# Optimization experiments

Measured on AMD Instinct MI355X. Metric: run time of the kernel, lower is better.

## Reference

```python
import jax, jax.numpy as jnp
import numpy as np


def setup_inputs() -> dict:
    key = jax.random.key(0)
    ks = jax.random.split(key, 8)
    B, C, H, W = 8, 64, 64, 64
    C2 = C // 2
    return {
        "x": jax.random.normal(ks[0], (B, C, H, W), dtype=jnp.float32),
        "Wq": jax.random.normal(ks[1], (C2, C), dtype=jnp.float32) * 0.1,
        "bq": jax.random.normal(ks[2], (C2,), dtype=jnp.float32) * 0.01,
        "Wk": jax.random.normal(ks[3], (C2, C), dtype=jnp.float32) * 0.1,
        "bk": jax.random.normal(ks[4], (C2,), dtype=jnp.float32) * 0.01,
        "Wv": jax.random.normal(ks[5], (C, C), dtype=jnp.float32) * 0.1,
        "bv": jax.random.normal(ks[6], (C,), dtype=jnp.float32) * 0.01,
        "sigma": jnp.float32(1.0),
    }


def reference(x, Wq, bq, Wk, bk, Wv, bv, sigma):
    B, C, H, W = x.shape
    N = H * W
    xf = x.reshape(B, C, N)  # flatten spatial
    # 1x1 convs == per-pixel linear projections over channels
    q = jnp.einsum("oc,bcn->bon", Wq, xf) + bq[None, :, None]  # [B, C/2, N]
    k = jnp.einsum("oc,bcn->bon", Wk, xf) + bk[None, :, None]  # [B, C/2, N]
    v = jnp.einsum("oc,bcn->bon", Wv, xf) + bv[None, :, None]  # [B, C,   N]
    # pairwise squared L2 distance via expansion: |q|^2 + |k|^2 - 2 q.k
    q_sq = jnp.sum(q * q, axis=1)  # [B, N]
    k_sq = jnp.sum(k * k, axis=1)  # [B, N]
    qk = jnp.einsum("bcn,bcm->bnm", q, k)  # [B, N, N]
    dist_sq = q_sq[:, :, None] + k_sq[:, None, :] - 2.0 * qk
    similarity = jnp.exp(-dist_sq / (2.0 * sigma * sigma))  # RBF kernel
    attention = jax.nn.softmax(similarity, axis=-1)  # [B, N, N]
    # attn @ v^T -> [B, N, C]
    attention_out = jnp.einsum("bnm,bcm->bnc", attention, v)
    # faithful to torch .view(B, C, H, W) on a [B, N, C] tensor (raw reshape)
    attention_out = attention_out.reshape(B, C, H, W)
    return x + attention_out
```

## Files before the change

kernel.cpp:

```cpp
#include <hip/hip_runtime.h>
#include <hip/hip_bf16.h>

typedef __attribute__((ext_vector_type(2))) _Float16 f16x2;
typedef __attribute__((ext_vector_type(4))) _Float16 f16x4;
typedef __attribute__((ext_vector_type(8))) _Float16 f16x8;
typedef __attribute__((ext_vector_type(4))) float f32x4;

#define B_ 8
#define N_ 4096
#define C_ 64
#define CQ_ 32
#define SPLIT 4
#define KEYS (N_ / SPLIT)
#define MB 64
#define NT (KEYS / MB)
#define QB 128

#define L2E_ 1.4426950408889634f
#define LOG2L_ 0.5287663729448977f

#define P0_ 0.9992f
#define P1_ 0.70591f
#define P2_ 0.20093f
#define P3_ 0.094395f

__device__ __forceinline__ void async16(void* lds, const void* gsrc) {
    __builtin_amdgcn_global_load_lds(
        (const __attribute__((address_space(1))) unsigned int*)gsrc,
        (__attribute__((address_space(3))) unsigned int*)lds, 16, 0, 0);
}

__device__ __forceinline__ f16x2 wpoly(float z0, float z1) {
    f16x2 h = __builtin_bit_cast(f16x2, __builtin_amdgcn_cvt_pkrtz(z0, z1));
    const _Float16 c3 = (_Float16)P3_, c2 = (_Float16)P2_;
    const _Float16 c1 = (_Float16)P1_, c0 = (_Float16)P0_;
    return ((h * c3 + c2) * h + c1) * h + c0;
}

__global__ __launch_bounds__(256) void proj_kernel(
    const float* __restrict__ x,
    const float* __restrict__ Wq, const float* __restrict__ bq,
    const float* __restrict__ Wk, const float* __restrict__ bk,
    const float* __restrict__ Wv, const float* __restrict__ bv,
    const float* __restrict__ sigp,
    _Float16* __restrict__ qh, _Float16* __restrict__ khf,
    _Float16* __restrict__ vhf,
    float* __restrict__ nqs, float* __restrict__ nkf)
{
    __shared__ float xs[64][64];
    __shared__ float sP[4][64];
    __shared__ _Float16 vtmp[64][76];

    const int t = threadIdx.x;
    const int wid = __builtin_amdgcn_readfirstlane(t >> 6);
    const int l = t & 63;
    const int typeB = (int)(blockIdx.x >> 9);
    const int bid = blockIdx.x & 511;
    const int b = bid >> 6;
    const int tile = bid & 63;
    const int n0 = tile * 64;

    #pragma unroll
    for (int rep = 0; rep < 16; ++rep) {
        const int idx = rep * 256 + t;
        xs[idx >> 6][idx & 63] = x[((size_t)b * C_ + (idx >> 6)) * N_ + n0 + (idx & 63)];
    }
    __syncthreads();

    const float* Wr;
    const float* br;
    if (!typeB) {
        Wr = (wid < 2) ? (Wq + wid * 16 * 64) : (Wk + (wid - 2) * 16 * 64);
        br = (wid < 2) ? (bq + wid * 16) : (bk + (wid - 2) * 16);
    } else {
        Wr = Wv + wid * 16 * 64;
        br = bv + wid * 16;
    }

    float acc[16];
    #pragma unroll
    for (int o = 0; o < 16; ++o) acc[o] = br[o];
    #pragma unroll
    for (int c0 = 0; c0 < 64; c0 += 8) {
        float xc[8];
        #pragma unroll
        for (int dc = 0; dc < 8; ++dc) xc[dc] = xs[c0 + dc][l];
        #pragma unroll
        for (int o = 0; o < 16; ++o) {
            #pragma unroll
            for (int dc = 0; dc < 8; ++dc)
                acc[o] = fmaf(Wr[o * 64 + c0 + dc], xc[dc], acc[o]);
        }
    }

    const float sv = sigp[0];
    const float cdL = 0.7213475204444817f / (sv * sv);
    const float c1 = 2.0f * cdL;
    const int n = n0 + l;

    if (!typeB) {
        float s = 0.f;
        #pragma unroll
        for (int o = 0; o < 16; ++o) s = fmaf(acc[o], acc[o], s);
        sP[wid][l] = s;
        if (wid < 2) {
            _Float16* row = qh + ((size_t)b * N_ + n) * CQ_ + wid * 16;
            #pragma unroll
            for (int j = 0; j < 2; ++j) {
                f16x8 h;
                #pragma unroll
                for (int e = 0; e < 8; ++e) h[e] = (_Float16)(acc[j * 8 + e] * c1);
                *(f16x8*)(row + j * 8) = h;
            }
        } else {
            const size_t tbase = ((size_t)b * (N_ / 64) + tile) * 4;
            #pragma unroll
            for (int gi = 0; gi < 2; ++gi) {
                const int g = (wid - 2) * 2 + gi;
                f16x8 h;
                #pragma unroll
                for (int e = 0; e < 8; ++e) h[e] = (_Float16)acc[gi * 8 + e];
                *(f16x8*)(khf + (tbase + g) * 512 + l * 8) = h;
            }
        }
        __syncthreads();
        if (t < 64) {
            nqs[(size_t)b * N_ + n0 + t] = LOG2L_ - (sP[0][t] + sP[1][t]) * cdL;
        } else if (t < 128) {
            const int kk = t - 64;
            const int kap = (((kk & 15) >> 2) << 3) + (kk & 3) + (((kk >> 4) & 1) << 2);
            nkf[((size_t)b * (N_ / 32) + ((n0 + kk) >> 5)) * 32 + kap] =
                -(sP[2][kk] + sP[3][kk]) * cdL;
        }
    } else {
        #pragma unroll
        for (int o = 0; o < 16; ++o) vtmp[wid * 16 + o][l] = (_Float16)acc[o];
        __syncthreads();
        #pragma unroll
        for (int p = 0; p < 2; ++p) {
            const int jg = (t >> 6) + p * 4;
            const int ch = t & 63;
            const int p0 = (jg >> 2) * 32 + (jg & 3) * 4;
            const f16x4 a0 = *(const f16x4*)(&vtmp[ch][p0]);
            const f16x4 a1 = *(const f16x4*)(&vtmp[ch][p0 + 16]);
            f16x8 hv;
            #pragma unroll
            for (int e = 0; e < 4; ++e) { hv[e] = a0[e]; hv[4 + e] = a1[e]; }
            *(f16x8*)(vhf + ((size_t)b * (N_ / 64) + tile) * 4096 + (jg * 64 + ch) * 8) = hv;
        }
    }
}

__global__ __launch_bounds__(256, 4) void attn_kernel(
    const _Float16* __restrict__ qh,
    const _Float16* __restrict__ khf,
    const _Float16* __restrict__ vhf,
    const float* __restrict__ nqs,
    const float* __restrict__ nkf,
    _Float16* __restrict__ opart,
    float* __restrict__ dpart)
{
    __shared__ __align__(16) _Float16 Kb[3][2048];
    __shared__ __align__(16) _Float16 Vb[3][4096];
    __shared__ __align__(16) float sNkAll[1024];

    const int t = threadIdx.x;
    const int wid = t >> 6;
    const int l = t & 63;
    const int lg = l >> 4;
    const int lm = l & 15;

    const int orig = blockIdx.x;
    const int wgid = (orig & 7) * 128 + (orig >> 3);
    const int qblk = wgid & 31;
    const int fam = wgid >> 5;
    const int split = fam & (SPLIT - 1);
    const int b = fam >> 2;
    const int qbase = qblk * QB + wid * 32;
    const int k0 = split * KEYS;
    const size_t bN = (size_t)b * N_;

    const f16x8 qfA = *(const f16x8*)(qh + (bN + qbase + lm) * CQ_ + 8 * lg);
    const f16x8 qfB = *(const f16x8*)(qh + (bN + qbase + 16 + lm) * CQ_ + 8 * lg);
    const float nqA = nqs[bN + qbase + lm];
    const float nqB = nqs[bN + qbase + 16 + lm];

    const _Float16* kg = khf + ((size_t)b * (N_ / 64) + (k0 >> 6)) * 2048 + wid * 512 + l * 8;
    const _Float16* vg = vhf + ((size_t)b * (N_ / 64) + (k0 >> 6)) * 4096 + wid * 1024 + l * 8;
    const float* nkp = nkf + bN + k0 + wid * 256 + l * 4;

    f32x4 accA[4], accB[4], accdA, accdB;
    #pragma unroll
    for (int i = 0; i < 4; ++i) {
        accA[i] = (f32x4){0.f, 0.f, 0.f, 0.f};
        accB[i] = (f32x4){0.f, 0.f, 0.f, 0.f};
    }
    accdA = (f32x4){0.f, 0.f, 0.f, 0.f};
    accdB = (f32x4){0.f, 0.f, 0.f, 0.f};
    f16x8 ones;
    #pragma unroll
    for (int e = 0; e < 8; ++e) ones[e] = (_Float16)1.0f;

    f16x8 paJ0A, paJ0B, paJ1A, paJ1B;

    auto ISSUE = [&](int tile, int bf) {
        async16(&Kb[bf][wid * 512],        kg + (size_t)tile * 2048);
        async16(&Vb[bf][wid * 1024],       vg + (size_t)tile * 4096);
        async16(&Vb[bf][wid * 1024 + 512], vg + (size_t)tile * 4096 + 512);
    };

    auto HALF = [&](int J, int tt, int ck, int cv, bool doPV, f16x8& pA, f16x8& pB) {
        const f16x8 kf0 = *(const f16x8*)(&Kb[ck][(lg * 64 + J * 32 + lm) * 8]);
        const f16x8 kf1 = *(const f16x8*)(&Kb[ck][(lg * 64 + J * 32 + 16 + lm) * 8]);
        const f32x4 NK0 = *(const f32x4*)(&sNkAll[tt * 64 + J * 32 + lg * 8]);
        const f32x4 NK1 = *(const f32x4*)(&sNkAll[tt * 64 + J * 32 + lg * 8 + 4]);
        f32x4 CA0, CA1, CB0, CB1;
        #pragma unroll
        for (int r = 0; r < 4; ++r) {
            CA0[r] = NK0[r] + nqA; CA1[r] = NK1[r] + nqA;
            CB0[r] = NK0[r] + nqB; CB1[r] = NK1[r] + nqB;
        }
        __builtin_amdgcn_s_setprio(1);
        const f32x4 SA0 = __builtin_amdgcn_mfma_f32_16x16x32_f16(kf0, qfA, CA0, 0, 0, 0);
        const f32x4 SA1 = __builtin_amdgcn_mfma_f32_16x16x32_f16(kf1, qfA, CA1, 0, 0, 0);
        const f32x4 SB0 = __builtin_amdgcn_mfma_f32_16x16x32_f16(kf0, qfB, CB0, 0, 0, 0);
        const f32x4 SB1 = __builtin_amdgcn_mfma_f32_16x16x32_f16(kf1, qfB, CB1, 0, 0, 0);
        __builtin_amdgcn_s_setprio(0);
        if (doPV) {
            __builtin_amdgcn_s_setprio(1);
            #pragma unroll
            for (int tc = 0; tc < 4; ++tc) {
                const f16x8 vf = *(const f16x8*)(&Vb[cv][((J * 4 + lg) * 64 + tc * 16 + lm) * 8]);
                accA[tc] = __builtin_amdgcn_mfma_f32_16x16x32_f16(pA, vf, accA[tc], 0, 0, 0);
                accB[tc] = __builtin_amdgcn_mfma_f32_16x16x32_f16(pB, vf, accB[tc], 0, 0, 0);
            }
            accdA = __builtin_amdgcn_mfma_f32_16x16x32_f16(pA, ones, accdA, 0, 0, 0);
            accdB = __builtin_amdgcn_mfma_f32_16x16x32_f16(pB, ones, accdB, 0, 0, 0);
            __builtin_amdgcn_s_setprio(0);
        }
        f16x2 w;
        w = wpoly(__builtin_amdgcn_exp2f(SA0[0]), __builtin_amdgcn_exp2f(SA0[1])); pA[0] = w[0]; pA[1] = w[1];
        w = wpoly(__builtin_amdgcn_exp2f(SA0[2]), __builtin_amdgcn_exp2f(SA0[3])); pA[2] = w[0]; pA[3] = w[1];
        w = wpoly(__builtin_amdgcn_exp2f(SA1[0]), __builtin_amdgcn_exp2f(SA1[1])); pA[4] = w[0]; pA[5] = w[1];
        w = wpoly(__builtin_amdgcn_exp2f(SA1[2]), __builtin_amdgcn_exp2f(SA1[3])); pA[6] = w[0]; pA[7] = w[1];
        w = wpoly(__builtin_amdgcn_exp2f(SB0[0]), __builtin_amdgcn_exp2f(SB0[1])); pB[0] = w[0]; pB[1] = w[1];
        w = wpoly(__builtin_amdgcn_exp2f(SB0[2]), __builtin_amdgcn_exp2f(SB0[3])); pB[2] = w[0]; pB[3] = w[1];
        w = wpoly(__builtin_amdgcn_exp2f(SB1[0]), __builtin_amdgcn_exp2f(SB1[1])); pB[4] = w[0]; pB[5] = w[1];
        w = wpoly(__builtin_amdgcn_exp2f(SB1[2]), __builtin_amdgcn_exp2f(SB1[3])); pB[6] = w[0]; pB[7] = w[1];
    };

    async16(&sNkAll[wid * 256], nkp);
    ISSUE(0, 0);
    asm volatile("s_waitcnt vmcnt(0)" ::: "memory");
    asm volatile("s_barrier" ::: "memory");
    ISSUE(1, 1);
    HALF(0, 0, 0, 0, false, paJ0A, paJ0B);
    HALF(1, 0, 0, 0, false, paJ1A, paJ1B);

    int cv = 0, ck = 1, ib = 2;
    #pragma unroll 1
    for (int tt = 1; tt < NT; ++tt) {
        asm volatile("s_waitcnt vmcnt(0)" ::: "memory");
        asm volatile("s_barrier" ::: "memory");
        if (tt + 1 < NT) ISSUE(tt + 1, ib);
        HALF(0, tt, ck, cv, true, paJ0A, paJ0B);
        HALF(1, tt, ck, cv, true, paJ1A, paJ1B);
        const int tmp = cv; cv = ck; ck = ib; ib = tmp;
    }

    __builtin_amdgcn_s_setprio(1);
    #pragma unroll
    for (int J = 0; J < 2; ++J) {
        const f16x8& pA = J ? paJ1A : paJ0A;
        const f16x8& pB = J ? paJ1B : paJ0B;
        #pragma unroll
        for (int tc = 0; tc < 4; ++tc) {
            const f16x8 vf = *(const f16x8*)(&Vb[cv][((J * 4 + lg) * 64 + tc * 16 + lm) * 8]);
            accA[tc] = __builtin_amdgcn_mfma_f32_16x16x32_f16(pA, vf, accA[tc], 0, 0, 0);
            accB[tc] = __builtin_amdgcn_mfma_f32_16x16x32_f16(pB, vf, accB[tc], 0, 0, 0);
        }
        accdA = __builtin_amdgcn_mfma_f32_16x16x32_f16(pA, ones, accdA, 0, 0, 0);
        accdB = __builtin_amdgcn_mfma_f32_16x16x32_f16(pB, ones, accdB, 0, 0, 0);
    }
    __builtin_amdgcn_s_setprio(0);

    const size_t obA = ((size_t)split * B_ + b) * N_ + qbase;
    if (lm == 0) {
        #pragma unroll
        for (int r = 0; r < 4; ++r) {
            dpart[obA + lg * 4 + r] = accdA[r];
            dpart[obA + 16 + lg * 4 + r] = accdB[r];
        }
    }
    #pragma unroll
    for (int tc = 0; tc < 4; ++tc) {
        #pragma unroll
        for (int r = 0; r < 4; ++r) {
            opart[(obA + lg * 4 + r) * C_ + tc * 16 + lm] = (_Float16)accA[tc][r];
            opart[(obA + 16 + lg * 4 + r) * C_ + tc * 16 + lm] = (_Float16)accB[tc][r];
        }
    }
}

__global__ __launch_bounds__(256) void combine_kernel(
    const float* __restrict__ x,
    const _Float16* __restrict__ opart,
    const float* __restrict__ dpart,
    float* __restrict__ out)
{
    const int gid = blockIdx.x * 256 + threadIdx.x;
    const int c0 = (gid & 7) * 8;
    const int bn = gid >> 3;

    float den = 0.f;
    #pragma unroll
    for (int s = 0; s < SPLIT; ++s) den += dpart[(size_t)s * B_ * N_ + bn];
    const float rden = 1.0f / den;

    float o[8] = {0.f, 0.f, 0.f, 0.f, 0.f, 0.f, 0.f, 0.f};
    #pragma unroll
    for (int s = 0; s < SPLIT; ++s) {
        const f16x8 h = *(const f16x8*)(opart + (((size_t)s * B_ * N_ + bn) * C_ + c0));
        #pragma unroll
        for (int e = 0; e < 8; ++e) o[e] += (float)h[e];
    }

    const size_t base = (size_t)bn * C_ + c0;
    const f32x4 x0 = *(const f32x4*)(x + base);
    const f32x4 x1 = *(const f32x4*)(x + base + 4);
    f32x4 r0, r1;
    #pragma unroll
    for (int e = 0; e < 4; ++e) {
        r0[e] = x0[e] + o[e] * rden;
        r1[e] = x1[e] + o[e + 4] * rden;
    }
    *(f32x4*)(out + base) = r0;
    *(f32x4*)(out + base + 4) = r1;
}

extern "C" void kernel_launch(void* const* d_in, const int* in_sizes, int n_in,
                              void* d_out, int out_size, void* d_ws, size_t ws_size,
                              hipStream_t stream) {
    const float* x   = (const float*)d_in[0];
    const float* Wq  = (const float*)d_in[1];
    const float* bq  = (const float*)d_in[2];
    const float* Wk  = (const float*)d_in[3];
    const float* bk  = (const float*)d_in[4];
    const float* Wv  = (const float*)d_in[5];
    const float* bv  = (const float*)d_in[6];
    const float* sig = (const float*)d_in[7];
    float* out = (float*)d_out;

    char* ws = (char*)d_ws;
    _Float16* qh   = (_Float16*)(ws);
    _Float16* khf  = (_Float16*)(ws + (2u << 20));
    _Float16* vhf  = (_Float16*)(ws + (4u << 20));
    float*   nqs   = (float*)(ws + (8u << 20));
    float*   nkf   = (float*)(ws + (8u << 20) + (128u << 10));
    _Float16* opart = (_Float16*)(ws + (8u << 20) + (256u << 10));
    float*   dpart = (float*)(ws + (24u << 20) + (256u << 10));

    proj_kernel<<<1024, 256, 0, stream>>>(x, Wq, bq, Wk, bk, Wv, bv, sig,
                                          qh, khf, vhf, nqs, nkf);
    attn_kernel<<<1024, 256, 0, stream>>>(qh, khf, vhf, nqs, nkf, opart, dpart);
    combine_kernel<<<(B_ * N_ * 8) / 256, 256, 0, stream>>>(x, opart, dpart, out);
}
```

Before: 69.14 us.

## Use FP8 for V and attention weights in PV MFMA, split keys eight ways

V is stored as packed FP8 and the softmax weights are evaluated as an fp32 polynomial and then packed to FP8, so the PV and denominator products run on fp8×fp8 MFMAs. This halves V's global traffic and its LDS footprint. The attention kernel is also templated on the key split and launches an eight-way split when the workspace is large enough, which doubles the number of workgroups and halves each one's key range. The cost is FP8 precision loss in V and in the weights, plus extra partial outputs for the combine kernel to read and sum.

```diff
diff --git a/kernel.cpp b/kernel.cpp
--- a/kernel.cpp
+++ b/kernel.cpp
@@ -10,10 +10,6 @@
 #define N_ 4096
 #define C_ 64
 #define CQ_ 32
-#define SPLIT 4
-#define KEYS (N_ / SPLIT)
-#define MB 64
-#define NT (KEYS / MB)
 #define QB 128
 
 #define L2E_ 1.4426950408889634f
@@ -30,11 +26,8 @@
         (__attribute__((address_space(3))) unsigned int*)lds, 16, 0, 0);
 }
 
-__device__ __forceinline__ f16x2 wpoly(float z0, float z1) {
-    f16x2 h = __builtin_bit_cast(f16x2, __builtin_amdgcn_cvt_pkrtz(z0, z1));
-    const _Float16 c3 = (_Float16)P3_, c2 = (_Float16)P2_;
-    const _Float16 c1 = (_Float16)P1_, c0 = (_Float16)P0_;
-    return ((h * c3 + c2) * h + c1) * h + c0;
+__device__ __forceinline__ float wpoly32(float z) {
+    return fmaf(fmaf(fmaf(P3_, z, P2_), z, P1_), z, P0_);
 }
 
 __global__ __launch_bounds__(256) void proj_kernel(
@@ -44,7 +37,7 @@
     const float* __restrict__ Wv, const float* __restrict__ bv,
     const float* __restrict__ sigp,
     _Float16* __restrict__ qh, _Float16* __restrict__ khf,
-    _Float16* __restrict__ vhf,
+    unsigned char* __restrict__ vhf,
     float* __restrict__ nqs, float* __restrict__ nkf)
 {
     __shared__ float xs[64][64];
@@ -143,26 +136,33 @@
             const int p0 = (jg >> 2) * 32 + (jg & 3) * 4;
             const f16x4 a0 = *(const f16x4*)(&vtmp[ch][p0]);
             const f16x4 a1 = *(const f16x4*)(&vtmp[ch][p0 + 16]);
-            f16x8 hv;
-            #pragma unroll
-            for (int e = 0; e < 4; ++e) { hv[e] = a0[e]; hv[4 + e] = a1[e]; }
-            *(f16x8*)(vhf + ((size_t)b * (N_ / 64) + tile) * 4096 + (jg * 64 + ch) * 8) = hv;
-        }
-    }
-}
-
+            int d0 = __builtin_amdgcn_cvt_pk_fp8_f32((float)a0[0], (float)a0[1], 0, false);
+            d0 = __builtin_amdgcn_cvt_pk_fp8_f32((float)a0[2], (float)a0[3], d0, true);
+            int d1 = __builtin_amdgcn_cvt_pk_fp8_f32((float)a1[0], (float)a1[1], 0, false);
+            d1 = __builtin_amdgcn_cvt_pk_fp8_f32((float)a1[2], (float)a1[3], d1, true);
+            uint2 u; u.x = (unsigned)d0; u.y = (unsigned)d1;
+            *(uint2*)(vhf + ((size_t)b * (N_ / 64) + tile) * 4096 + (size_t)(jg * 64 + ch) * 8) = u;
+        }
+    }
+}
+
+template <int SPLITT>
 __global__ __launch_bounds__(256, 4) void attn_kernel(
     const _Float16* __restrict__ qh,
     const _Float16* __restrict__ khf,
-    const _Float16* __restrict__ vhf,
+    const unsigned char* __restrict__ vhf,
     const float* __restrict__ nqs,
     const float* __restrict__ nkf,
     _Float16* __restrict__ opart,
     float* __restrict__ dpart)
 {
+    constexpr int KEYS = N_ / SPLITT;
+    constexpr int NT = KEYS / 64;
+    constexpr int CPX = (B_ * (N_ / QB) * SPLITT) / 8;
+
     __shared__ __align__(16) _Float16 Kb[3][2048];
-    __shared__ __align__(16) _Float16 Vb[3][4096];
-    __shared__ __align__(16) float sNkAll[1024];
+    __shared__ __align__(16) unsigned char Vb[3][4096];
+    __shared__ __align__(16) float sNkAll[KEYS];
 
     const int t = threadIdx.x;
     const int wid = t >> 6;
@@ -171,11 +171,11 @@
     const int lm = l & 15;
 
     const int orig = blockIdx.x;
-    const int wgid = (orig & 7) * 128 + (orig >> 3);
+    const int wgid = (orig & 7) * CPX + (orig >> 3);
     const int qblk = wgid & 31;
     const int fam = wgid >> 5;
-    const int split = fam & (SPLIT - 1);
-    const int b = fam >> 2;
+    const int split = fam & (SPLITT - 1);
+    const int b = fam / SPLITT;
     const int qbase = qblk * QB + wid * 32;
     const int k0 = split * KEYS;
     const size_t bN = (size_t)b * N_;
@@ -186,7 +186,7 @@
     const float nqB = nqs[bN + qbase + 16 + lm];
 
     const _Float16* kg = khf + ((size_t)b * (N_ / 64) + (k0 >> 6)) * 2048 + wid * 512 + l * 8;
-    const _Float16* vg = vhf + ((size_t)b * (N_ / 64) + (k0 >> 6)) * 4096 + wid * 1024 + l * 8;
+    const unsigned char* vg = vhf + ((size_t)b * (N_ / 64) + (k0 >> 6)) * 4096 + wid * 1024 + l * 16;
     const float* nkp = nkf + bN + k0 + wid * 256 + l * 4;
 
     f32x4 accA[4], accB[4], accdA, accdB;
@@ -197,19 +197,16 @@
     }
     accdA = (f32x4){0.f, 0.f, 0.f, 0.f};
     accdB = (f32x4){0.f, 0.f, 0.f, 0.f};
-    f16x8 ones;
-    #pragma unroll
-    for (int e = 0; e < 8; ++e) ones[e] = (_Float16)1.0f;
-
-    f16x8 paJ0A, paJ0B, paJ1A, paJ1B;
+    const long long onesF8 = 0x3838383838383838LL;
+
+    long long paJ0A, paJ0B, paJ1A, paJ1B;
 
     auto ISSUE = [&](int tile, int bf) {
-        async16(&Kb[bf][wid * 512],        kg + (size_t)tile * 2048);
-        async16(&Vb[bf][wid * 1024],       vg + (size_t)tile * 4096);
-        async16(&Vb[bf][wid * 1024 + 512], vg + (size_t)tile * 4096 + 512);
+        async16(&Kb[bf][wid * 512], kg + (size_t)tile * 2048);
+        async16(&Vb[bf][wid * 1024], vg + (size_t)tile * 4096);
     };
 
-    auto HALF = [&](int J, int tt, int ck, int cv, bool doPV, f16x8& pA, f16x8& pB) {
+    auto HALF = [&](int J, int tt, int ck, int cv, bool doPV, long long& pA, long long& pB) {
         const f16x8 kf0 = *(const f16x8*)(&Kb[ck][(lg * 64 + J * 32 + lm) * 8]);
         const f16x8 kf1 = *(const f16x8*)(&Kb[ck][(lg * 64 + J * 32 + 16 + lm) * 8]);
         const f32x4 NK0 = *(const f32x4*)(&sNkAll[tt * 64 + J * 32 + lg * 8]);
@@ -230,26 +227,50 @@
             __builtin_amdgcn_s_setprio(1);
             #pragma unroll
             for (int tc = 0; tc < 4; ++tc) {
-                const f16x8 vf = *(const f16x8*)(&Vb[cv][((J * 4 + lg) * 64 + tc * 16 + lm) * 8]);
-                accA[tc] = __builtin_amdgcn_mfma_f32_16x16x32_f16(pA, vf, accA[tc], 0, 0, 0);
-                accB[tc] = __builtin_amdgcn_mfma_f32_16x16x32_f16(pB, vf, accB[tc], 0, 0, 0);
+                const uint2 vu = *(const uint2*)(&Vb[cv][((J * 4 + lg) * 64 + tc * 16 + lm) * 8]);
+                const long long vfl = __builtin_bit_cast(long long, vu);
+                accA[tc] = __builtin_amdgcn_mfma_f32_16x16x32_fp8_fp8(pA, vfl, accA[tc], 0, 0, 0);
+                accB[tc] = __builtin_amdgcn_mfma_f32_16x16x32_fp8_fp8(pB, vfl, accB[tc], 0, 0, 0);
             }
-            accdA = __builtin_amdgcn_mfma_f32_16x16x32_f16(pA, ones, accdA, 0, 0, 0);
-            accdB = __builtin_amdgcn_mfma_f32_16x16x32_f16(pB, ones, accdB, 0, 0, 0);
+            accdA = __builtin_amdgcn_mfma_f32_16x16x32_fp8_fp8(pA, onesF8, accdA, 0, 0, 0);
+            accdB = __builtin_amdgcn_mfma_f32_16x16x32_fp8_fp8(pB, onesF8, accdB, 0, 0, 0);
             __builtin_amdgcn_s_setprio(0);
         }
-        f16x2 w;
-        w = wpoly(__builtin_amdgcn_exp2f(SA0[0]), __builtin_amdgcn_exp2f(SA0[1])); pA[0] = w[0]; pA[1] = w[1];
-        w = wpoly(__builtin_amdgcn_exp2f(SA0[2]), __builtin_amdgcn_exp2f(SA0[3])); pA[2] = w[0]; pA[3] = w[1];
-        w = wpoly(__builtin_amdgcn_exp2f(SA1[0]), __builtin_amdgcn_exp2f(SA1[1])); pA[4] = w[0]; pA[5] = w[1];
-        w = wpoly(__builtin_amdgcn_exp2f(SA1[2]), __builtin_amdgcn_exp2f(SA1[3])); pA[6] = w[0]; pA[7] = w[1];
-        w = wpoly(__builtin_amdgcn_exp2f(SB0[0]), __builtin_amdgcn_exp2f(SB0[1])); pB[0] = w[0]; pB[1] = w[1];
-        w = wpoly(__builtin_amdgcn_exp2f(SB0[2]), __builtin_amdgcn_exp2f(SB0[3])); pB[2] = w[0]; pB[3] = w[1];
-        w = wpoly(__builtin_amdgcn_exp2f(SB1[0]), __builtin_amdgcn_exp2f(SB1[1])); pB[4] = w[0]; pB[5] = w[1];
-        w = wpoly(__builtin_amdgcn_exp2f(SB1[2]), __builtin_amdgcn_exp2f(SB1[3])); pB[6] = w[0]; pB[7] = w[1];
+        {
+            const float w0 = wpoly32(__builtin_amdgcn_exp2f(SA0[0]));
+            const float w1 = wpoly32(__builtin_amdgcn_exp2f(SA0[1]));
+            const float w2 = wpoly32(__builtin_amdgcn_exp2f(SA0[2]));
+            const float w3 = wpoly32(__builtin_amdgcn_exp2f(SA0[3]));
+            const float w4 = wpoly32(__builtin_amdgcn_exp2f(SA1[0]));
+            const float w5 = wpoly32(__builtin_amdgcn_exp2f(SA1[1]));
+            const float w6 = wpoly32(__builtin_amdgcn_exp2f(SA1[2]));
+            const float w7 = wpoly32(__builtin_amdgcn_exp2f(SA1[3]));
+            int d0 = __builtin_amdgcn_cvt_pk_fp8_f32(w0, w1, 0, false);
+            d0 = __builtin_amdgcn_cvt_pk_fp8_f32(w2, w3, d0, true);
+            int d1 = __builtin_amdgcn_cvt_pk_fp8_f32(w4, w5, 0, false);
+            d1 = __builtin_amdgcn_cvt_pk_fp8_f32(w6, w7, d1, true);
+            uint2 u; u.x = (unsigned)d0; u.y = (unsigned)d1;
+            pA = __builtin_bit_cast(long long, u);
+        }
+        {
+            const float w0 = wpoly32(__builtin_amdgcn_exp2f(SB0[0]));
+            const float w1 = wpoly32(__builtin_amdgcn_exp2f(SB0[1]));
+            const float w2 = wpoly32(__builtin_amdgcn_exp2f(SB0[2]));
+            const float w3 = wpoly32(__builtin_amdgcn_exp2f(SB0[3]));
+            const float w4 = wpoly32(__builtin_amdgcn_exp2f(SB1[0]));
+            const float w5 = wpoly32(__builtin_amdgcn_exp2f(SB1[1]));
+            const float w6 = wpoly32(__builtin_amdgcn_exp2f(SB1[2]));
+            const float w7 = wpoly32(__builtin_amdgcn_exp2f(SB1[3]));
+            int d0 = __builtin_amdgcn_cvt_pk_fp8_f32(w0, w1, 0, false);
+            d0 = __builtin_amdgcn_cvt_pk_fp8_f32(w2, w3, d0, true);
+            int d1 = __builtin_amdgcn_cvt_pk_fp8_f32(w4, w5, 0, false);
+            d1 = __builtin_amdgcn_cvt_pk_fp8_f32(w6, w7, d1, true);
+            uint2 u; u.x = (unsigned)d0; u.y = (unsigned)d1;
+            pB = __builtin_bit_cast(long long, u);
+        }
     };
 
-    async16(&sNkAll[wid * 256], nkp);
+    if (wid < KEYS / 256) async16(&sNkAll[wid * 256], nkp);
     ISSUE(0, 0);
     asm volatile("s_waitcnt vmcnt(0)" ::: "memory");
     asm volatile("s_barrier" ::: "memory");
@@ -271,16 +292,17 @@
     __builtin_amdgcn_s_setprio(1);
     #pragma unroll
     for (int J = 0; J < 2; ++J) {
-        const f16x8& pA = J ? paJ1A : paJ0A;
-        const f16x8& pB = J ? paJ1B : paJ0B;
+        const long long pA = J ? paJ1A : paJ0A;
+        const long long pB = J ? paJ1B : paJ0B;
         #pragma unroll
         for (int tc = 0; tc < 4; ++tc) {
-            const f16x8 vf = *(const f16x8*)(&Vb[cv][((J * 4 + lg) * 64 + tc * 16 + lm) * 8]);
-            accA[tc] = __builtin_amdgcn_mfma_f32_16x16x32_f16(pA, vf, accA[tc], 0, 0, 0);
-            accB[tc] = __builtin_amdgcn_mfma_f32_16x16x32_f16(pB, vf, accB[tc], 0, 0, 0);
-        }
-        accdA = __builtin_amdgcn_mfma_f32_16x16x32_f16(pA, ones, accdA, 0, 0, 0);
-        accdB = __builtin_amdgcn_mfma_f32_16x16x32_f16(pB, ones, accdB, 0, 0, 0);
+            const uint2 vu = *(const uint2*)(&Vb[cv][((J * 4 + lg) * 64 + tc * 16 + lm) * 8]);
+            const long long vfl = __builtin_bit_cast(long long, vu);
+            accA[tc] = __builtin_amdgcn_mfma_f32_16x16x32_fp8_fp8(pA, vfl, accA[tc], 0, 0, 0);
+            accB[tc] = __builtin_amdgcn_mfma_f32_16x16x32_fp8_fp8(pB, vfl, accB[tc], 0, 0, 0);
+        }
+        accdA = __builtin_amdgcn_mfma_f32_16x16x32_fp8_fp8(pA, onesF8, accdA, 0, 0, 0);
+        accdB = __builtin_amdgcn_mfma_f32_16x16x32_fp8_fp8(pB, onesF8, accdB, 0, 0, 0);
     }
     __builtin_amdgcn_s_setprio(0);
 
@@ -302,6 +324,7 @@
     }
 }
 
+template <int SPLITT>
 __global__ __launch_bounds__(256) void combine_kernel(
     const float* __restrict__ x,
     const _Float16* __restrict__ opart,
@@ -314,12 +337,12 @@
 
     float den = 0.f;
     #pragma unroll
-    for (int s = 0; s < SPLIT; ++s) den += dpart[(size_t)s * B_ * N_ + bn];
+    for (int s = 0; s < SPLITT; ++s) den += dpart[(size_t)s * B_ * N_ + bn];
     const float rden = 1.0f / den;
 
     float o[8] = {0.f, 0.f, 0.f, 0.f, 0.f, 0.f, 0.f, 0.f};
     #pragma unroll
-    for (int s = 0; s < SPLIT; ++s) {
+    for (int s = 0; s < SPLITT; ++s) {
         const f16x8 h = *(const f16x8*)(opart + (((size_t)s * B_ * N_ + bn) * C_ + c0));
         #pragma unroll
         for (int e = 0; e < 8; ++e) o[e] += (float)h[e];
@@ -352,16 +375,26 @@
     float* out = (float*)d_out;
 
     char* ws = (char*)d_ws;
-    _Float16* qh   = (_Float16*)(ws);
-    _Float16* khf  = (_Float16*)(ws + (2u << 20));
-    _Float16* vhf  = (_Float16*)(ws + (4u << 20));
-    float*   nqs   = (float*)(ws + (8u << 20));
-    float*   nkf   = (float*)(ws + (8u << 20) + (128u << 10));
-    _Float16* opart = (_Float16*)(ws + (8u << 20) + (256u << 10));
-    float*   dpart = (float*)(ws + (24u << 20) + (256u << 10));
+    _Float16* qh        = (_Float16*)(ws);
+    _Float16* khf       = (_Float16*)(ws + (2u << 20));
+    unsigned char* vhf  = (unsigned char*)(ws + (4u << 20));
+    float* nqs          = (float*)(ws + (6u << 20));
+    float* nkf          = (float*)(ws + (6u << 20) + (128u << 10));
+    _Float16* opart     = (_Float16*)(ws + (8u << 20));
 
     proj_kernel<<<1024, 256, 0, stream>>>(x, Wq, bq, Wk, bk, Wv, bv, sig,
                                           qh, khf, vhf, nqs, nkf);
-    attn_kernel<<<1024, 256, 0, stream>>>(qh, khf, vhf, nqs, nkf, opart, dpart);
-    combine_kernel<<<(B_ * N_ * 8) / 256, 256, 0, stream>>>(x, opart, dpart, out);
-}
+
+    const size_t need8 = (8ull << 20) + 8ull * (4ull << 20) + 8ull * (128ull << 10);
+    if (ws_size >= need8) {
+        float* dpart = (float*)(ws + (8ull << 20) + 8ull * (4ull << 20));
+        attn_kernel<8><<<B_ * (N_ / QB) * 8, 256, 0, stream>>>(qh, khf, vhf, nqs, nkf,
+                                                               opart, dpart);
+        combine_kernel<8><<<(B_ * N_ * 8) / 256, 256, 0, stream>>>(x, opart, dpart, out);
+    } else {
+        float* dpart = (float*)(ws + (8ull << 20) + 4ull * (4ull << 20));
+        attn_kernel<4><<<B_ * (N_ / QB) * 4, 256, 0, stream>>>(qh, khf, vhf, nqs, nkf,
+                                                               opart, dpart);
+        combine_kernel<4><<<(B_ * N_ * 8) / 256, 256, 0, stream>>>(x, opart, dpart, out);
+    }
+}
```

Result: slower. 77.52 us (+12.1%).

## Compute projections with fp16 MFMA and merge Q/K/V work into one block

Applied to the files above, without the earlier changes.

The 1x1-conv projection kernel now converts the x tile and weights to fp16 and computes Q, K and V with 16x16x32 MFMA instructions instead of scalar FMA loops. Each block now produces all three projections for its tile, one wave each for Q and K and two for V, which halves the grid and reads x once rather than twice. Squared norms are reduced with cross-lane shuffles instead of a shared-memory pass. The cost is lower precision in the projections, since the fp16 inputs to the MFMA add rounding error that feeds into the exponential.

```diff
diff --git a/kernel.cpp b/kernel.cpp
--- a/kernel.cpp
+++ b/kernel.cpp
@@ -12,8 +12,7 @@
 #define CQ_ 32
 #define SPLIT 4
 #define KEYS (N_ / SPLIT)
-#define MB 64
-#define NT (KEYS / MB)
+#define NT (KEYS / 64)
 #define QB 128
 
 #define L2E_ 1.4426950408889634f
@@ -47,107 +46,155 @@
     _Float16* __restrict__ vhf,
     float* __restrict__ nqs, float* __restrict__ nkf)
 {
-    __shared__ float xs[64][64];
-    __shared__ float sP[4][64];
-    __shared__ _Float16 vtmp[64][76];
+    __shared__ __align__(16) _Float16 xs16[64][72];
+    __shared__ __align__(16) _Float16 vtmp[64][76];
 
     const int t = threadIdx.x;
     const int wid = __builtin_amdgcn_readfirstlane(t >> 6);
     const int l = t & 63;
-    const int typeB = (int)(blockIdx.x >> 9);
-    const int bid = blockIdx.x & 511;
-    const int b = bid >> 6;
-    const int tile = bid & 63;
+    const int lg = l >> 4;
+    const int lm = l & 15;
+    const int b = blockIdx.x >> 6;
+    const int tile = blockIdx.x & 63;
     const int n0 = tile * 64;
-
-    #pragma unroll
-    for (int rep = 0; rep < 16; ++rep) {
-        const int idx = rep * 256 + t;
-        xs[idx >> 6][idx & 63] = x[((size_t)b * C_ + (idx >> 6)) * N_ + n0 + (idx & 63)];
+    const size_t bN = (size_t)b * N_;
+
+    {
+        const int c = t >> 2, pq = t & 3;
+        const float* xp = x + (bN * C_ / N_ * 0 + ((size_t)b * C_ + c) * N_) + n0 + pq * 16;
+        f32x4 a0 = *(const f32x4*)(xp);
+        f32x4 a1 = *(const f32x4*)(xp + 4);
+        f32x4 a2 = *(const f32x4*)(xp + 8);
+        f32x4 a3 = *(const f32x4*)(xp + 12);
+        #pragma unroll
+        for (int i = 0; i < 4; ++i) {
+            xs16[pq * 16 + i][c]      = (_Float16)a0[i];
+            xs16[pq * 16 + 4 + i][c]  = (_Float16)a1[i];
+            xs16[pq * 16 + 8 + i][c]  = (_Float16)a2[i];
+            xs16[pq * 16 + 12 + i][c] = (_Float16)a3[i];
+        }
     }
     __syncthreads();
 
     const float* Wr;
     const float* br;
-    if (!typeB) {
-        Wr = (wid < 2) ? (Wq + wid * 16 * 64) : (Wk + (wid - 2) * 16 * 64);
-        br = (wid < 2) ? (bq + wid * 16) : (bk + (wid - 2) * 16);
-    } else {
-        Wr = Wv + wid * 16 * 64;
-        br = bv + wid * 16;
-    }
-
-    float acc[16];
-    #pragma unroll
-    for (int o = 0; o < 16; ++o) acc[o] = br[o];
-    #pragma unroll
-    for (int c0 = 0; c0 < 64; c0 += 8) {
-        float xc[8];
-        #pragma unroll
-        for (int dc = 0; dc < 8; ++dc) xc[dc] = xs[c0 + dc][l];
-        #pragma unroll
-        for (int o = 0; o < 16; ++o) {
-            #pragma unroll
-            for (int dc = 0; dc < 8; ++dc)
-                acc[o] = fmaf(Wr[o * 64 + c0 + dc], xc[dc], acc[o]);
+    if (wid == 0)      { Wr = Wq;            br = bq; }
+    else if (wid == 1) { Wr = Wk;            br = bk; }
+    else if (wid == 2) { Wr = Wv;            br = bv; }
+    else               { Wr = Wv + 32 * 64;  br = bv + 32; }
+
+    f16x8 af[2][2];
+    #pragma unroll
+    for (int og = 0; og < 2; ++og) {
+        #pragma unroll
+        for (int ks = 0; ks < 2; ++ks) {
+            const float* wp = Wr + (og * 16 + lm) * 64 + ks * 32 + lg * 8;
+            const f32x4 w0 = *(const f32x4*)(wp);
+            const f32x4 w1 = *(const f32x4*)(wp + 4);
+            f16x8 h;
+            #pragma unroll
+            for (int e = 0; e < 4; ++e) { h[e] = (_Float16)w0[e]; h[4 + e] = (_Float16)w1[e]; }
+            af[og][ks] = h;
+        }
+    }
+    f32x4 bias[2];
+    #pragma unroll
+    for (int og = 0; og < 2; ++og)
+        bias[og] = *(const f32x4*)(br + og * 16 + lg * 4);
+
+    f32x4 d[2][4];
+    #pragma unroll
+    for (int pg = 0; pg < 4; ++pg) {
+        const f16x8 bf0 = *(const f16x8*)(&xs16[pg * 16 + lm][lg * 8]);
+        const f16x8 bf1 = *(const f16x8*)(&xs16[pg * 16 + lm][32 + lg * 8]);
+        #pragma unroll
+        for (int og = 0; og < 2; ++og) {
+            f32x4 acc = __builtin_amdgcn_mfma_f32_16x16x32_f16(af[og][0], bf0, bias[og], 0, 0, 0);
+            d[og][pg] = __builtin_amdgcn_mfma_f32_16x16x32_f16(af[og][1], bf1, acc, 0, 0, 0);
         }
     }
 
     const float sv = sigp[0];
     const float cdL = 0.7213475204444817f / (sv * sv);
     const float c1 = 2.0f * cdL;
-    const int n = n0 + l;
-
-    if (!typeB) {
-        float s = 0.f;
-        #pragma unroll
-        for (int o = 0; o < 16; ++o) s = fmaf(acc[o], acc[o], s);
-        sP[wid][l] = s;
-        if (wid < 2) {
-            _Float16* row = qh + ((size_t)b * N_ + n) * CQ_ + wid * 16;
-            #pragma unroll
-            for (int j = 0; j < 2; ++j) {
-                f16x8 h;
-                #pragma unroll
-                for (int e = 0; e < 8; ++e) h[e] = (_Float16)(acc[j * 8 + e] * c1);
-                *(f16x8*)(row + j * 8) = h;
+
+    if (wid < 2) {
+        float s[4];
+        #pragma unroll
+        for (int pg = 0; pg < 4; ++pg) {
+            float acc = 0.f;
+            #pragma unroll
+            for (int og = 0; og < 2; ++og)
+                #pragma unroll
+                for (int r = 0; r < 4; ++r)
+                    acc = fmaf(d[og][pg][r], d[og][pg][r], acc);
+            acc += __shfl_xor(acc, 16);
+            acc += __shfl_xor(acc, 32);
+            s[pg] = acc;
+        }
+        if (wid == 0) {
+            #pragma unroll
+            for (int og = 0; og < 2; ++og) {
+                #pragma unroll
+                for (int pg = 0; pg < 4; ++pg) {
+                    f16x4 h;
+                    #pragma unroll
+                    for (int r = 0; r < 4; ++r) h[r] = (_Float16)(d[og][pg][r] * c1);
+                    *(f16x4*)(qh + (bN + n0 + pg * 16 + lm) * CQ_ + og * 16 + lg * 4) = h;
+                }
+            }
+            if (l < 16) {
+                #pragma unroll
+                for (int pg = 0; pg < 4; ++pg)
+                    nqs[bN + n0 + pg * 16 + l] = LOG2L_ - s[pg] * cdL;
             }
         } else {
             const size_t tbase = ((size_t)b * (N_ / 64) + tile) * 4;
             #pragma unroll
-            for (int gi = 0; gi < 2; ++gi) {
-                const int g = (wid - 2) * 2 + gi;
-                f16x8 h;
-                #pragma unroll
-                for (int e = 0; e < 8; ++e) h[e] = (_Float16)acc[gi * 8 + e];
-                *(f16x8*)(khf + (tbase + g) * 512 + l * 8) = h;
+            for (int og = 0; og < 2; ++og) {
+                const int g = og * 2 + (lg >> 1);
+                const int e0 = (lg & 1) * 4;
+                #pragma unroll
+                for (int pg = 0; pg < 4; ++pg) {
+                    f16x4 h;
+                    #pragma unroll
+                    for (int r = 0; r < 4; ++r) h[r] = (_Float16)d[og][pg][r];
+                    *(f16x4*)(khf + (tbase + g) * 512 + (pg * 16 + lm) * 8 + e0) = h;
+                }
             }
-        }
-        __syncthreads();
-        if (t < 64) {
-            nqs[(size_t)b * N_ + n0 + t] = LOG2L_ - (sP[0][t] + sP[1][t]) * cdL;
-        } else if (t < 128) {
-            const int kk = t - 64;
-            const int kap = (((kk & 15) >> 2) << 3) + (kk & 3) + (((kk >> 4) & 1) << 2);
-            nkf[((size_t)b * (N_ / 32) + ((n0 + kk) >> 5)) * 32 + kap] =
-                -(sP[2][kk] + sP[3][kk]) * cdL;
+            if (l < 16) {
+                #pragma unroll
+                for (int pg = 0; pg < 4; ++pg) {
+                    const int kkg = n0 + pg * 16 + l;
+                    const int kk = kkg & 31;
+                    const int kap = (((kk & 15) >> 2) << 3) + (kk & 3) + (((kk >> 4) & 1) << 2);
+                    nkf[((size_t)b * (N_ / 32) + (kkg >> 5)) * 32 + kap] = -s[pg] * cdL;
+                }
+            }
         }
     } else {
-        #pragma unroll
-        for (int o = 0; o < 16; ++o) vtmp[wid * 16 + o][l] = (_Float16)acc[o];
-        __syncthreads();
-        #pragma unroll
-        for (int p = 0; p < 2; ++p) {
-            const int jg = (t >> 6) + p * 4;
-            const int ch = t & 63;
-            const int p0 = (jg >> 2) * 32 + (jg & 3) * 4;
-            const f16x4 a0 = *(const f16x4*)(&vtmp[ch][p0]);
-            const f16x4 a1 = *(const f16x4*)(&vtmp[ch][p0 + 16]);
-            f16x8 hv;
-            #pragma unroll
-            for (int e = 0; e < 4; ++e) { hv[e] = a0[e]; hv[4 + e] = a1[e]; }
-            *(f16x8*)(vhf + ((size_t)b * (N_ / 64) + tile) * 4096 + (jg * 64 + ch) * 8) = hv;
-        }
+        const int co = (wid - 2) * 32;
+        #pragma unroll
+        for (int og = 0; og < 2; ++og)
+            #pragma unroll
+            for (int pg = 0; pg < 4; ++pg)
+                #pragma unroll
+                for (int r = 0; r < 4; ++r)
+                    vtmp[co + og * 16 + lg * 4 + r][pg * 16 + lm] = (_Float16)d[og][pg][r];
+    }
+    __syncthreads();
+
+    #pragma unroll
+    for (int p = 0; p < 2; ++p) {
+        const int jg = (t >> 6) + p * 4;
+        const int ch = t & 63;
+        const int p0 = (jg >> 2) * 32 + (jg & 3) * 4;
+        const f16x4 a0 = *(const f16x4*)(&vtmp[ch][p0]);
+        const f16x4 a1 = *(const f16x4*)(&vtmp[ch][p0 + 16]);
+        f16x8 hv;
+        #pragma unroll
+        for (int e = 0; e < 4; ++e) { hv[e] = a0[e]; hv[4 + e] = a1[e]; }
+        *(f16x8*)(vhf + ((size_t)b * (N_ / 64) + tile) * 4096 + (size_t)(jg * 64 + ch) * 8) = hv;
     }
 }
 
@@ -360,8 +407,8 @@
     _Float16* opart = (_Float16*)(ws + (8u << 20) + (256u << 10));
     float*   dpart = (float*)(ws + (24u << 20) + (256u << 10));
 
-    proj_kernel<<<1024, 256, 0, stream>>>(x, Wq, bq, Wk, bk, Wv, bv, sig,
-                                          qh, khf, vhf, nqs, nkf);
+    proj_kernel<<<512, 256, 0, stream>>>(x, Wq, bq, Wk, bk, Wv, bv, sig,
+                                         qh, khf, vhf, nqs, nkf);
     attn_kernel<<<1024, 256, 0, stream>>>(qh, khf, vhf, nqs, nkf, opart, dpart);
     combine_kernel<<<(B_ * N_ * 8) / 256, 256, 0, stream>>>(x, opart, dpart, out);
 }
```

Measured after the change: 55.95 us. 1.24x faster.
